# Optimization experiments

Measured on AMD Instinct MI355X. Metric: run time of the kernel, lower is better.

Reference implementation:

```python
import jax, jax.numpy as jnp
import numpy as np

B, N = 64, 4096          # trees per batch, leaves per complete binary tree
V, S = 21, 50            # amino-acid vocab, grammar-symbol vocab
E, H = 64, 128           # embed_dim, hidden_dim


def setup_inputs() -> dict:
    key = jax.random.key(0)
    ks = jax.random.split(key, 16)

    def lin_w(k, din, dout):
        return (jax.random.normal(k, (dout, din), jnp.float32) / np.sqrt(din)).astype(jnp.float32)

    tokens = jax.random.randint(ks[0], (B, N), 0, V, dtype=jnp.int32)
    symbols = jax.random.randint(ks[1], (B, N - 1), 0, S, dtype=jnp.int32)

    emb = jax.random.normal(ks[2], (V, E), jnp.float32) * 0.02
    emb = emb.at[0].set(0.0)  # padding_idx=0
    sym_emb = jax.random.normal(ks[3], (S, E), jnp.float32) * 0.02

    return {
        "tokens": tokens, "symbols": symbols,
        "emb": emb, "sym_emb": sym_emb,
        "Wp": lin_w(ks[4], E, H), "bp": jnp.zeros((H,), jnp.float32),
        "Wi": lin_w(ks[5], H, H), "bi": jnp.zeros((H,), jnp.float32),
        "Ui": lin_w(ks[6], H, H),
        "Wf": lin_w(ks[7], H, H), "bf": jnp.zeros((H,), jnp.float32),
        "Uf": lin_w(ks[8], H, H),
        "Wo": lin_w(ks[9], H, H), "bo": jnp.zeros((H,), jnp.float32),
        "Uo": lin_w(ks[10], H, H),
        "Wu": lin_w(ks[11], H, H), "bu": jnp.zeros((H,), jnp.float32),
        "Uu": lin_w(ks[12], H, H),
        "Wout": lin_w(ks[13], H, H), "bout": jnp.zeros((H,), jnp.float32),
    }


def _encode(tokens, symbols, emb, sym_emb, Wp, bp, Wi, bi, Ui, Wf, bf, Uf,
            Wo, bo, Uo, Wu, bu, Uu, Wout, bout):
    emb = emb.at[0].set(0.0)  # padding row contributes nothing (and gets no grad)

    # Leaf nodes: amino-acid embedding -> input_proj, no children.
    x = emb[tokens] @ Wp.T + bp                      # [B, N, H]
    i = jax.nn.sigmoid(x @ Wi.T + bi)
    o = jax.nn.sigmoid(x @ Wo.T + bo)
    u = jnp.tanh(x @ Wu.T + bu)
    c = i * u                                        # [B, N, H]
    h = o * jnp.tanh(c)

    # Bottom-up over levels of the complete binary tree (Child-Sum Tree-LSTM).
    off, n = 0, N
    while n > 1:
        m = n // 2
        xs = sym_emb[symbols[:, off:off + m]] @ Wp.T + bp   # [B, m, H]
        hl, hr = h[:, 0::2], h[:, 1::2]
        cl, cr = c[:, 0::2], c[:, 1::2]
        ht = hl + hr                                         # h_tilde = sum_j h_j
        gi = jax.nn.sigmoid(xs @ Wi.T + bi + ht @ Ui.T)
        go = jax.nn.sigmoid(xs @ Wo.T + bo + ht @ Uo.T)
        gu = jnp.tanh(xs @ Wu.T + bu + ht @ Uu.T)
        fx = xs @ Wf.T + bf
        fl = jax.nn.sigmoid(fx + hl @ Uf.T)                  # per-child forget gates
        fr = jax.nn.sigmoid(fx + hr @ Uf.T)
        c = gi * gu + fl * cl + fr * cr
        h = go * jnp.tanh(c)
        off += m
        n = m

    root_h = h[:, 0]                                         # [B, H]
    return root_h @ Wout.T + bout                            # output_proj


def reference(tokens, symbols, emb, sym_emb, Wp, bp, Wi, bi, Ui, Wf, bf, Uf,
              Wo, bo, Uo, Wu, bu, Uu, Wout, bout):
    return _encode(tokens, symbols, emb, sym_emb, Wp, bp, Wi, bi, Ui, Wf, bf,
                   Uf, Wo, bo, Uo, Wu, bu, Uu, Wout, bout)
```

## Files before the change

### kernel.cpp

```cpp
#include <hip/hip_runtime.h>
#include <hip/hip_bf16.h>

typedef __attribute__((ext_vector_type(8))) short short8;
typedef __attribute__((ext_vector_type(4))) float f32x4;

static constexpr int B_ = 64;
static constexpr int N_ = 4096;
static constexpr int V_ = 21;
static constexpr int S_ = 50;
static constexpr int E_ = 64;
static constexpr int H_ = 128;
static constexpr int NPAIR = V_ * V_;
static constexpr int NTAB = NPAIR * S_;

__device__ __forceinline__ float rcp_(float x) { return __builtin_amdgcn_rcpf(x); }
__device__ __forceinline__ float sigm(float x) { return rcp_(1.0f + __expf(-x)); }
__device__ __forceinline__ float tanh_(float x) {
  float a = fabsf(x);
  float e = __expf(-2.0f * a);
  float t = (1.0f - e) * rcp_(1.0f + e);
  return x < 0.0f ? -t : t;
}
__device__ __forceinline__ unsigned short f2bf(float f) {
  __hip_bfloat16 b = __float2bfloat16(f);
  return *reinterpret_cast<unsigned short*>(&b);
}
__device__ __forceinline__ float bf2f(unsigned short u) {
  return __uint_as_float(((unsigned int)u) << 16);
}

struct Gates { float cv, hv; };
__device__ __forceinline__ Gates gate_combine(float4 sx,
    float i_p, float o_p, float u_p, float fl_p, float fr_p, float cl, float cr) {
  float gi = sigm(sx.x + i_p);
  float go = sigm(sx.y + o_p);
  float gu = tanh_(sx.z + u_p);
  float fl = sigm(sx.w + fl_p);
  float fr = sigm(sx.w + fr_p);
  float cv = fmaf(gi, gu, fmaf(fl, cl, fr * cr));
  Gates g; g.cv = cv; g.hv = go * tanh_(cv);
  return g;
}

__global__ void __launch_bounds__(512) k_pre0(
    const float* __restrict__ Ui, const float* __restrict__ Uo,
    const float* __restrict__ Uu, const float* __restrict__ Uf,
    const float* __restrict__ Wi, const float* __restrict__ Wo,
    const float* __restrict__ Wu, const float* __restrict__ Wf,
    const float* __restrict__ Wp, const float* __restrict__ Wout,
    unsigned short* __restrict__ Wfrag, float* __restrict__ Wt,
    float* __restrict__ Wxt, float* __restrict__ Wpt,
    float* __restrict__ Woutt) {
  __shared__ float Tt[32][129];
  int blk = blockIdx.x, t = threadIdx.x;
  if (blk < 16) {
    int idx = blk * 512 + t;
    int L = idx & 63;
    int K = (idx >> 6) & 3;
    int T = idx >> 8;
    int n = 16 * T + (L & 15);
    int k0 = 32 * K + ((L >> 4) << 3);
    int g = n >> 7, o = n & 127;
    const float* U = (g == 0) ? Ui : (g == 1) ? Uo : (g == 2) ? Uu : Uf;
    unsigned short out[8];
    #pragma unroll
    for (int j = 0; j < 8; ++j) out[j] = f2bf(U[o * 128 + k0 + j]);
    *(int4*)(Wfrag + (size_t)idx * 8) = *(int4*)out;
  } else if (blk < 48) {
    int job = blk - 16;
    int m = job >> 2, kt = job & 3;
    int k0 = kt * 32;
    const float* M = (m == 0) ? Ui : (m == 1) ? Uo : (m == 2) ? Uu : (m == 3) ? Uf
                   : (m == 4) ? Wi : (m == 5) ? Wo : (m == 6) ? Wu : Wf;
    float* D = (m < 4) ? Wt : Wxt;
    int g = m & 3;
    #pragma unroll
    for (int pass = 0; pass < 2; ++pass) {
      int o = (t >> 3) + 64 * pass;
      int kk = 4 * (t & 7);
      float4 v = *(const float4*)(M + o * 128 + k0 + kk);
      Tt[kk][o] = v.x; Tt[kk + 1][o] = v.y; Tt[kk + 2][o] = v.z; Tt[kk + 3][o] = v.w;
    }
    __syncthreads();
    #pragma unroll
    for (int pass = 0; pass < 8; ++pass) {
      int kk = pass * 4 + (t >> 7);
      int o = t & 127;
      D[(size_t)(k0 + kk) * 512 + g * 128 + o] = Tt[kk][o];
    }
  } else if (blk == 48) {
    for (int i = t; i < E_ * H_; i += 512) {
      int e = i >> 7, o = i & 127;
      Wpt[i] = Wp[o * E_ + e];
    }
  } else {
    for (int i = t; i < H_ * H_; i += 512) {
      int k = i >> 7, o = i & 127;
      Woutt[i] = Wout[o * H_ + k];
    }
  }
}

__global__ void __launch_bounds__(512) k_pre1(
    const float* __restrict__ emb, const float* __restrict__ sym_emb,
    const float* __restrict__ Wpt, const float* __restrict__ Wxt,
    const float* __restrict__ Wt,
    const float* __restrict__ bp, const float* __restrict__ bi,
    const float* __restrict__ bo, const float* __restrict__ bu,
    const float* __restrict__ bfv,
    unsigned short* __restrict__ leaf_h8, float* __restrict__ leaf_c,
    float* __restrict__ symx, float* __restrict__ P_leaf) {
  __shared__ float x[128];
  __shared__ float zs[512];
  __shared__ float hl[128];
  int blk = blockIdx.x, t = threadIdx.x;
  if (blk < V_) {
    int v = blk;
    if (t < 128) {
      float acc = bp[t];
      if (v != 0) {
        for (int e = 0; e < E_; ++e) acc = fmaf(emb[v * E_ + e], Wpt[e * 128 + t], acc);
      }
      x[t] = acc;
    }
    __syncthreads();
    if (t < 384) {
      int g = t >> 7;
      const float* bb = (g == 0) ? bi : (g == 1) ? bo : bu;
      float z = bb[t & 127];
      for (int k = 0; k < H_; ++k) z = fmaf(x[k], Wxt[k * 512 + t], z);
      zs[t] = z;
    }
    __syncthreads();
    if (t < 128) {
      float gi = sigm(zs[t]), go = sigm(zs[128 + t]), gu = tanh_(zs[256 + t]);
      float c = gi * gu;
      leaf_c[v * H_ + t] = c;
      unsigned short hb = f2bf(go * tanh_(c));
      leaf_h8[v * H_ + t] = hb;
      hl[t] = bf2f(hb);
    }
    __syncthreads();
    {
      float z = 0.f;
      for (int k = 0; k < H_; ++k) z = fmaf(hl[k], Wt[k * 512 + t], z);
      P_leaf[(size_t)v * 512 + t] = z;
    }
  } else {
    int s = blk - V_;
    if (t < 128) {
      float acc = bp[t];
      for (int e = 0; e < E_; ++e) acc = fmaf(sym_emb[s * E_ + e], Wpt[e * 128 + t], acc);
      x[t] = acc;
    }
    __syncthreads();
    {
      int g = t >> 7;
      const float* bb = (g == 0) ? bi : (g == 1) ? bo : (g == 2) ? bu : bfv;
      float z = bb[t & 127];
      for (int k = 0; k < H_; ++k) z = fmaf(x[k], Wxt[k * 512 + t], z);
      zs[t] = z;
    }
    __syncthreads();
    if (t < 128) {
      float4 v4 = make_float4(zs[t], zs[128 + t], zs[256 + t], zs[384 + t]);
      *(float4*)(symx + (size_t)s * 512 + t * 4) = v4;
    }
  }
}

__global__ void k_tabB(const float* __restrict__ P_leaf, const float* __restrict__ symx,
                       const float* __restrict__ leaf_c,
                       const int* __restrict__ tokens, const int* __restrict__ symbols,
                       unsigned short* __restrict__ tab_h8, float* __restrict__ tab_c,
                       int* __restrict__ idx1) {
  int blk = blockIdx.x, t = threadIdx.x;
  if (blk < NTAB / 2) {
    int row = blk * 2 + (t >> 7);
    int u = t & 127;
    int p = row / S_, s = row - p * S_;
    int tl = p / V_, tr = p - tl * V_;
    const float* Pl = P_leaf + (size_t)tl * 512;
    const float* Pr = P_leaf + (size_t)tr * 512;
    float4 sx = *(const float4*)(symx + (size_t)s * 512 + u * 4);
    Gates gt = gate_combine(sx,
        Pl[u] + Pr[u], Pl[128 + u] + Pr[128 + u], Pl[256 + u] + Pr[256 + u],
        Pl[384 + u], Pr[384 + u],
        leaf_c[tl * H_ + u], leaf_c[tr * H_ + u]);
    tab_c[(size_t)row * H_ + u] = gt.cv;
    tab_h8[(size_t)row * H_ + u] = f2bf(gt.hv);
  } else {
    int g = (blk - NTAB / 2) * 256 + t;
    int b = g >> 11, j = g & 2047;
    idx1[g] = (tokens[b * N_ + 2 * j] * V_ + tokens[b * N_ + 2 * j + 1]) * S_ + symbols[b * (N_ - 1) + j];
  }
}

__global__ void __launch_bounds__(512, 4) k_lvl23(
    const unsigned short* __restrict__ Wfrag, const float* __restrict__ symx,
    const int* __restrict__ symbols, const int* __restrict__ idx1,
    const unsigned short* __restrict__ gh8, const float* __restrict__ gc,
    unsigned short* __restrict__ h_out8, float* __restrict__ c_out) {
  __shared__ __align__(16) unsigned short Ag[64][136];
  __shared__ __align__(16) unsigned short Bh[32][136];
  __shared__ float Bc[32][132];
  int t = threadIdx.x;
  int w = t >> 6, L = t & 63, q = L >> 4, cL = L & 15;
  int cc = 16 * w + cL;
  int g0 = blockIdx.x * 32;
  int b = g0 >> 10;
  int j2 = g0 & 1023;
  const int* sym_b = symbols + (size_t)b * (N_ - 1);
  const int* gix = idx1 + 2 * g0;

  #pragma unroll
  for (int i = 0; i < 2; ++i) {
    int fid = t + 512 * i;
    int row = fid >> 4, co = (fid & 15) * 8;
    *(int4*)&Ag[row][co] = *(const int4*)(gh8 + (size_t)gix[row] * H_ + co);
  }
  __syncthreads();

  const short8* wf = (const short8*)Wfrag;
  #pragma unroll
  for (int c = 0; c < 2; ++c) {
    float clp[4], crp[4];
    int spre[4];
    #pragma unroll
    for (int it = 0; it < 4; ++it) {
      int n = 16 * c + 8 * (it >> 1) + 2 * q + (it & 1);
      clp[it] = gc[(size_t)gix[2 * n] * H_ + cc];
      crp[it] = gc[(size_t)gix[2 * n + 1] * H_ + cc];
      spre[it] = sym_b[2048 + j2 + n];
    }
    f32x4 acc[2][4];
    #pragma unroll
    for (int r = 0; r < 2; ++r)
      #pragma unroll
      for (int g = 0; g < 4; ++g) acc[r][g] = (f32x4){0.f, 0.f, 0.f, 0.f};
    #pragma unroll
    for (int K = 0; K < 4; ++K) {
      short8 bfr[4];
      #pragma unroll
      for (int g = 0; g < 4; ++g) bfr[g] = wf[(size_t)((w + 8 * g) * 4 + K) * 64 + L];
      short8 a0 = *(const short8*)&Ag[32 * c + cL][K * 32 + q * 8];
      short8 a1 = *(const short8*)&Ag[32 * c + 16 + cL][K * 32 + q * 8];
      #pragma unroll
      for (int g = 0; g < 4; ++g) {
        acc[0][g] = __builtin_amdgcn_mfma_f32_16x16x32_bf16(a0, bfr[g], acc[0][g], 0, 0, 0);
        acc[1][g] = __builtin_amdgcn_mfma_f32_16x16x32_bf16(a1, bfr[g], acc[1][g], 0, 0, 0);
      }
    }
    #pragma unroll
    for (int r = 0; r < 2; ++r) {
      #pragma unroll
      for (int nd = 0; nd < 2; ++nd) {
        int it = r * 2 + nd;
        int n = 16 * c + 8 * r + 2 * q + nd;
        float4 sx = *(const float4*)(symx + (size_t)spre[it] * 512 + cc * 4);
        Gates gt = gate_combine(sx,
            acc[r][0][2 * nd] + acc[r][0][2 * nd + 1],
            acc[r][1][2 * nd] + acc[r][1][2 * nd + 1],
            acc[r][2][2 * nd] + acc[r][2][2 * nd + 1],
            acc[r][3][2 * nd], acc[r][3][2 * nd + 1], clp[it], crp[it]);
        Bc[n][cc] = gt.cv;
        Bh[n][cc] = f2bf(gt.hv);
      }
    }
  }
  __syncthreads();
  {
    int spre[4];
    #pragma unroll
    for (int it = 0; it < 4; ++it) {
      int n = 8 * (it >> 1) + 2 * q + (it & 1);
      spre[it] = sym_b[3072 + (j2 >> 1) + n];
    }
    f32x4 acc[2][4];
    #pragma unroll
    for (int r = 0; r < 2; ++r)
      #pragma unroll
      for (int g = 0; g < 4; ++g) acc[r][g] = (f32x4){0.f, 0.f, 0.f, 0.f};
    #pragma unroll
    for (int K = 0; K < 4; ++K) {
      short8 bfr[4];
      #pragma unroll
      for (int g = 0; g < 4; ++g) bfr[g] = wf[(size_t)((w + 8 * g) * 4 + K) * 64 + L];
      short8 a0 = *(const short8*)&Bh[cL][K * 32 + q * 8];
      short8 a1 = *(const short8*)&Bh[16 + cL][K * 32 + q * 8];
      #pragma unroll
      for (int g = 0; g < 4; ++g) {
        acc[0][g] = __builtin_amdgcn_mfma_f32_16x16x32_bf16(a0, bfr[g], acc[0][g], 0, 0, 0);
        acc[1][g] = __builtin_amdgcn_mfma_f32_16x16x32_bf16(a1, bfr[g], acc[1][g], 0, 0, 0);
      }
    }
    #pragma unroll
    for (int r = 0; r < 2; ++r) {
      #pragma unroll
      for (int nd = 0; nd < 2; ++nd) {
        int it = r * 2 + nd;
        int n = 8 * r + 2 * q + nd;
        int G3 = (g0 >> 1) + n;
        float4 sx = *(const float4*)(symx + (size_t)spre[it] * 512 + cc * 4);
        Gates gt = gate_combine(sx,
            acc[r][0][2 * nd] + acc[r][0][2 * nd + 1],
            acc[r][1][2 * nd] + acc[r][1][2 * nd + 1],
            acc[r][2][2 * nd] + acc[r][2][2 * nd + 1],
            acc[r][3][2 * nd], acc[r][3][2 * nd + 1],
            Bc[2 * n][cc], Bc[2 * n + 1][cc]);
        c_out[(size_t)G3 * H_ + cc] = gt.cv;
        h_out8[(size_t)G3 * H_ + cc] = f2bf(gt.hv);
      }
    }
  }
}

__global__ void __launch_bounds__(512, 2) k_mid(
    const unsigned short* __restrict__ Wfrag, const float* __restrict__ symx,
    const int* __restrict__ symbols,
    const unsigned short* __restrict__ in_h8, const float* __restrict__ in_c,
    unsigned short* __restrict__ out_h8, float* __restrict__ out_c) {
  __shared__ __align__(16) unsigned short Ah0[64][136];
  __shared__ __align__(16) unsigned short Ah1[32][136];
  __shared__ float Cs0[64][128];
  __shared__ float Cs1[32][128];
  int t = threadIdx.x;
  int w = t >> 6, L = t & 63, q = L >> 4, cL = L & 15;
  int cc = 16 * w + cL;
  int blk = blockIdx.x;
  int b = blk >> 3, sub = blk & 7;
  size_t base3 = (size_t)blk * 64;

  #pragma unroll
  for (int i = 0; i < 2; ++i) {
    int fid = t + 512 * i;
    int row = fid >> 4, co = (fid & 15) * 8;
    *(int4*)&Ah0[row][co] = *(const int4*)(in_h8 + (base3 + row) * H_ + co);
  }
  #pragma unroll
  for (int i = 0; i < 4; ++i) {
    int fid = t + 512 * i;
    int row = fid >> 5, c4 = (fid & 31) << 2;
    *(float4*)&Cs0[row][c4] = *(const float4*)(in_c + (base3 + row) * H_ + c4);
  }
  __syncthreads();

  const short8* wf = (const short8*)Wfrag;
  int R = 64;
  #pragma unroll
  for (int lev = 0; lev < 6; ++lev) {
    const int l = 4 + lev;
    const int nodes = R >> 1;
    const int jb = b * (N_ - 1) + (N_ - (N_ >> (l - 1))) + ((sub * 32) >> lev);
    unsigned short (*Ard)[136] = (lev & 1) ? Ah1 : Ah0;
    unsigned short (*Awr)[136] = (lev & 1) ? Ah0 : Ah1;
    const float* crd = (lev & 1) ? &Cs1[0][0] : &Cs0[0][0];
    float* cwr = (lev & 1) ? &Cs0[0][0] : &Cs1[0][0];
    const int nchunk = (nodes + 15) >> 4;
    for (int c = 0; c < nchunk; ++c) {
      int spre[4];
      #pragma unroll
      for (int it = 0; it < 4; ++it) {
        int n = 16 * c + 8 * (it >> 1) + 2 * q + (it & 1);
        spre[it] = (n < nodes) ? symbols[jb + n] : 0;
      }
      f32x4 acc[2][4];
      #pragma unroll
      for (int r = 0; r < 2; ++r)
        #pragma unroll
        for (int g = 0; g < 4; ++g) acc[r][g] = (f32x4){0.f, 0.f, 0.f, 0.f};
      const bool useA1 = (2 * nodes - 32 * c) > 16;
      #pragma unroll
      for (int K = 0; K < 4; ++K) {
        short8 bfr[4];
        #pragma unroll
        for (int g = 0; g < 4; ++g) bfr[g] = wf[(size_t)((w + 8 * g) * 4 + K) * 64 + L];
        short8 a0 = *(const short8*)&Ard[32 * c + cL][K * 32 + q * 8];
        #pragma unroll
        for (int g = 0; g < 4; ++g)
          acc[0][g] = __builtin_amdgcn_mfma_f32_16x16x32_bf16(a0, bfr[g], acc[0][g], 0, 0, 0);
        if (useA1) {
          short8 a1 = *(const short8*)&Ard[32 * c + 16 + cL][K * 32 + q * 8];
          #pragma unroll
          for (int g = 0; g < 4; ++g)
            acc[1][g] = __builtin_amdgcn_mfma_f32_16x16x32_bf16(a1, bfr[g], acc[1][g], 0, 0, 0);
        }
      }
      #pragma unroll
      for (int r = 0; r < 2; ++r) {
        #pragma unroll
        for (int nd = 0; nd < 2; ++nd) {
          int it = r * 2 + nd;
          int n = 16 * c + 8 * r + 2 * q + nd;
          if (n < nodes) {
            float4 sx = *(const float4*)(symx + (size_t)spre[it] * 512 + cc * 4);
            Gates gt = gate_combine(sx,
                acc[r][0][2 * nd] + acc[r][0][2 * nd + 1],
                acc[r][1][2 * nd] + acc[r][1][2 * nd + 1],
                acc[r][2][2 * nd] + acc[r][2][2 * nd + 1],
                acc[r][3][2 * nd], acc[r][3][2 * nd + 1],
                crd[(size_t)(2 * n) * 128 + cc], crd[(size_t)(2 * n + 1) * 128 + cc]);
            if (lev == 5) {
              out_c[(size_t)blk * H_ + cc] = gt.cv;
              out_h8[(size_t)blk * H_ + cc] = f2bf(gt.hv);
            } else {
              cwr[(size_t)n * 128 + cc] = gt.cv;
              Awr[n][cc] = f2bf(gt.hv);
            }
          }
        }
      }
    }
    __syncthreads();
    R >>= 1;
  }
}

__global__ void __launch_bounds__(512, 2) k_fin(
    const unsigned short* __restrict__ Wfrag, const float* __restrict__ symx,
    const int* __restrict__ symbols,
    const unsigned short* __restrict__ in_h8, const float* __restrict__ in_c,
    const float* __restrict__ Woutt, const float* __restrict__ bout,
    float* __restrict__ out) {
  __shared__ __align__(16) unsigned short Ah0[8][136];
  __shared__ __align__(16) unsigned short Ah1[4][136];
  __shared__ float Cs0[8][128];
  __shared__ float Cs1[4][128];
  __shared__ float rootv[128];
  int t = threadIdx.x;
  int w = t >> 6, L = t & 63, q = L >> 4, cL = L & 15;
  int cc = 16 * w + cL;
  int b = blockIdx.x;

  if (t < 128) {
    int row = t >> 4, co = (t & 15) * 8;
    *(int4*)&Ah0[row][co] = *(const int4*)(in_h8 + (size_t)(b * 8 + row) * H_ + co);
  }
  if (t < 256) {
    int row = t >> 5, c4 = (t & 31) << 2;
    *(float4*)&Cs0[row][c4] = *(const float4*)(in_c + (size_t)(b * 8 + row) * H_ + c4);
  }
  __syncthreads();

  const short8* wf = (const short8*)Wfrag;
  int R = 8;
  #pragma unroll
  for (int lev = 0; lev < 3; ++lev) {
    const int l = 10 + lev;
    const int nodes = R >> 1;
    const int jb = b * (N_ - 1) + (N_ - (N_ >> (l - 1)));
    unsigned short (*Ard)[136] = (lev & 1) ? Ah1 : Ah0;
    unsigned short (*Awr)[136] = (lev & 1) ? Ah0 : Ah1;
    const float* crd = (lev & 1) ? &Cs1[0][0] : &Cs0[0][0];
    float* cwr = (lev & 1) ? &Cs0[0][0] : &Cs1[0][0];
    int spre[4];
    #pragma unroll
    for (int it = 0; it < 4; ++it) {
      int n = 8 * (it >> 1) + 2 * q + (it & 1);
      spre[it] = (n < nodes) ? symbols[jb + n] : 0;
    }
    f32x4 acc[4];
    #pragma unroll
    for (int g = 0; g < 4; ++g) acc[g] = (f32x4){0.f, 0.f, 0.f, 0.f};
    #pragma unroll
    for (int K = 0; K < 4; ++K) {
      short8 bfr[4];
      #pragma unroll
      for (int g = 0; g < 4; ++g) bfr[g] = wf[(size_t)((w + 8 * g) * 4 + K) * 64 + L];
      short8 a0 = *(const short8*)&Ard[cL & 7][K * 32 + q * 8];
      #pragma unroll
      for (int g = 0; g < 4; ++g)
        acc[g] = __builtin_amdgcn_mfma_f32_16x16x32_bf16(a0, bfr[g], acc[g], 0, 0, 0);
    }
    #pragma unroll
    for (int nd = 0; nd < 2; ++nd) {
      int it = nd;
      int n = 2 * q + nd;
      if (n < nodes) {
        float4 sx = *(const float4*)(symx + (size_t)spre[it] * 512 + cc * 4);
        Gates gt = gate_combine(sx,
            acc[0][2 * nd] + acc[0][2 * nd + 1],
            acc[1][2 * nd] + acc[1][2 * nd + 1],
            acc[2][2 * nd] + acc[2][2 * nd + 1],
            acc[3][2 * nd], acc[3][2 * nd + 1],
            crd[(size_t)(2 * n) * 128 + cc], crd[(size_t)(2 * n + 1) * 128 + cc]);
        if (lev == 2) {
          rootv[cc] = gt.hv;
        } else {
          cwr[(size_t)n * 128 + cc] = gt.cv;
          Awr[n][cc] = f2bf(gt.hv);
        }
      }
    }
    __syncthreads();
    R >>= 1;
  }
  if (t < 128) {
    float acc = bout[t];
    for (int k = 0; k < H_; ++k) acc = fmaf(rootv[k], Woutt[k * 128 + t], acc);
    out[(size_t)b * H_ + t] = acc;
  }
}

extern "C" void kernel_launch(void* const* d_in, const int* in_sizes, int n_in,
                              void* d_out, int out_size, void* d_ws, size_t ws_size,
                              hipStream_t stream) {
  const int* tokens    = (const int*)d_in[0];
  const int* symbols   = (const int*)d_in[1];
  const float* emb     = (const float*)d_in[2];
  const float* sym_emb = (const float*)d_in[3];
  const float* Wp  = (const float*)d_in[4];
  const float* bp  = (const float*)d_in[5];
  const float* Wi  = (const float*)d_in[6];
  const float* bi  = (const float*)d_in[7];
  const float* Ui  = (const float*)d_in[8];
  const float* Wf  = (const float*)d_in[9];
  const float* bf  = (const float*)d_in[10];
  const float* Uf  = (const float*)d_in[11];
  const float* Wo  = (const float*)d_in[12];
  const float* bo  = (const float*)d_in[13];
  const float* Uo  = (const float*)d_in[14];
  const float* Wu  = (const float*)d_in[15];
  const float* bu  = (const float*)d_in[16];
  const float* Uu  = (const float*)d_in[17];
  const float* Wout= (const float*)d_in[18];
  const float* bout= (const float*)d_in[19];

  char* ws = (char*)d_ws;
  unsigned short* Wfrag   = (unsigned short*)(ws);
  float*          Wt      = (float*)(ws + 131072);
  float*          Wxt     = (float*)(ws + 393216);
  float*          Wpt     = (float*)(ws + 655360);
  float*          Woutt   = (float*)(ws + 688128);
  unsigned short* leaf_h8 = (unsigned short*)(ws + 753664);
  float*          leaf_c  = (float*)(ws + 759040);
  float*          symx    = (float*)(ws + 769792);
  float*          P_leaf  = (float*)(ws + 872192);
  unsigned short* tab_h8  = (unsigned short*)(ws + 2001152UL);
  float*          tab_c   = (float*)(ws + 7645952UL);
  int*            idx1    = (int*)(ws + 18935552UL);
  unsigned short* L3h8    = (unsigned short*)(ws + 19459840UL);
  float*          L3c     = (float*)(ws + 27848448UL);
  unsigned short* L9h8    = (unsigned short*)(ws + 44625664UL);
  float*          L9c     = (float*)(ws + 44756736UL);

  k_pre0<<<50, 512, 0, stream>>>(Ui, Uo, Uu, Uf, Wi, Wo, Wu, Wf, Wp, Wout,
                                 Wfrag, Wt, Wxt, Wpt, Woutt);
  k_pre1<<<V_ + S_, 512, 0, stream>>>(emb, sym_emb, Wpt, Wxt, Wt,
                                      bp, bi, bo, bu, bf,
                                      leaf_h8, leaf_c, symx, P_leaf);
  k_tabB<<<NTAB / 2 + 512, 256, 0, stream>>>(P_leaf, symx, leaf_c, tokens, symbols,
                                             tab_h8, tab_c, idx1);
  k_lvl23<<<2048, 512, 0, stream>>>(Wfrag, symx, symbols, idx1, tab_h8, tab_c, L3h8, L3c);
  k_mid<<<512, 512, 0, stream>>>(Wfrag, symx, symbols, L3h8, L3c, L9h8, L9c);
  k_fin<<<B_, 512, 0, stream>>>(Wfrag, symx, symbols, L9h8, L9c, Woutt, bout,
                                (float*)d_out);
}
```

Measured before the change: 216.2 us.

## Fuse preprocessing and table kernels with grid barrier; merge mid and final levels

Merges the weight-fragment, embedding projection, leaf/symbol precompute, and pair-table kernels into a single kernel that uses an atomic-counter grid barrier between phases. The transposed weight copies are dropped; the weights are read in their original row-major layout. The mid and final tree-level kernels are also merged, with the last 64 blocks waiting on a counter for all 512 blocks before running the top levels. This cuts launches and intermediate buffers, at the cost of spin-wait barriers that assume all blocks are co-resident, less coalesced weight reads, and a raised occupancy hint on the merged kernel.

```diff
diff --git a/kernel.cpp b/kernel.cpp
--- a/kernel.cpp
+++ b/kernel.cpp
@@ -42,19 +42,26 @@
   return g;
 }
 
-__global__ void __launch_bounds__(512) k_pre0(
-    const float* __restrict__ Ui, const float* __restrict__ Uo,
-    const float* __restrict__ Uu, const float* __restrict__ Uf,
-    const float* __restrict__ Wi, const float* __restrict__ Wo,
-    const float* __restrict__ Wu, const float* __restrict__ Wf,
-    const float* __restrict__ Wp, const float* __restrict__ Wout,
-    unsigned short* __restrict__ Wfrag, float* __restrict__ Wt,
-    float* __restrict__ Wxt, float* __restrict__ Wpt,
-    float* __restrict__ Woutt) {
-  __shared__ float Tt[32][129];
+__global__ void __launch_bounds__(256) k_pre_tab(
+    const float* __restrict__ emb, const float* __restrict__ sym_emb,
+    const float* __restrict__ Wp, const float* __restrict__ bp,
+    const float* __restrict__ Wi, const float* __restrict__ bi, const float* __restrict__ Ui,
+    const float* __restrict__ Wf, const float* __restrict__ bfv, const float* __restrict__ Uf,
+    const float* __restrict__ Wo, const float* __restrict__ bo, const float* __restrict__ Uo,
+    const float* __restrict__ Wu, const float* __restrict__ bu, const float* __restrict__ Uu,
+    const int* __restrict__ tokens, const int* __restrict__ symbols,
+    unsigned short* __restrict__ Wfrag,
+    unsigned short* __restrict__ leaf_h8, float* __restrict__ leaf_c,
+    float* __restrict__ symx, float* __restrict__ P_leaf,
+    unsigned short* __restrict__ tab_h8, float* __restrict__ tab_c,
+    int* __restrict__ idx1, unsigned int* __restrict__ ctr) {
+  __shared__ float x[128];
+  __shared__ float zs[512];
+  __shared__ float hsh[128];
   int blk = blockIdx.x, t = threadIdx.x;
-  if (blk < 16) {
-    int idx = blk * 512 + t;
+
+  if (blk < 32) {
+    int idx = blk * 256 + t;
     int L = idx & 63;
     int K = (idx >> 6) & 3;
     int T = idx >> 8;
@@ -66,70 +73,29 @@
     #pragma unroll
     for (int j = 0; j < 8; ++j) out[j] = f2bf(U[o * 128 + k0 + j]);
     *(int4*)(Wfrag + (size_t)idx * 8) = *(int4*)out;
-  } else if (blk < 48) {
-    int job = blk - 16;
-    int m = job >> 2, kt = job & 3;
-    int k0 = kt * 32;
-    const float* M = (m == 0) ? Ui : (m == 1) ? Uo : (m == 2) ? Uu : (m == 3) ? Uf
-                   : (m == 4) ? Wi : (m == 5) ? Wo : (m == 6) ? Wu : Wf;
-    float* D = (m < 4) ? Wt : Wxt;
-    int g = m & 3;
-    #pragma unroll
-    for (int pass = 0; pass < 2; ++pass) {
-      int o = (t >> 3) + 64 * pass;
-      int kk = 4 * (t & 7);
-      float4 v = *(const float4*)(M + o * 128 + k0 + kk);
-      Tt[kk][o] = v.x; Tt[kk + 1][o] = v.y; Tt[kk + 2][o] = v.z; Tt[kk + 3][o] = v.w;
-    }
-    __syncthreads();
-    #pragma unroll
-    for (int pass = 0; pass < 8; ++pass) {
-      int kk = pass * 4 + (t >> 7);
-      int o = t & 127;
-      D[(size_t)(k0 + kk) * 512 + g * 128 + o] = Tt[kk][o];
-    }
-  } else if (blk == 48) {
-    for (int i = t; i < E_ * H_; i += 512) {
-      int e = i >> 7, o = i & 127;
-      Wpt[i] = Wp[o * E_ + e];
-    }
-  } else {
-    for (int i = t; i < H_ * H_; i += 512) {
-      int k = i >> 7, o = i & 127;
-      Woutt[i] = Wout[o * H_ + k];
-    }
-  }
-}
-
-__global__ void __launch_bounds__(512) k_pre1(
-    const float* __restrict__ emb, const float* __restrict__ sym_emb,
-    const float* __restrict__ Wpt, const float* __restrict__ Wxt,
-    const float* __restrict__ Wt,
-    const float* __restrict__ bp, const float* __restrict__ bi,
-    const float* __restrict__ bo, const float* __restrict__ bu,
-    const float* __restrict__ bfv,
-    unsigned short* __restrict__ leaf_h8, float* __restrict__ leaf_c,
-    float* __restrict__ symx, float* __restrict__ P_leaf) {
-  __shared__ float x[128];
-  __shared__ float zs[512];
-  __shared__ float hl[128];
-  int blk = blockIdx.x, t = threadIdx.x;
-  if (blk < V_) {
-    int v = blk;
+  } else if (blk < 53) {
+    int v = blk - 32;
     if (t < 128) {
       float acc = bp[t];
       if (v != 0) {
-        for (int e = 0; e < E_; ++e) acc = fmaf(emb[v * E_ + e], Wpt[e * 128 + t], acc);
+        const float* wr = Wp + t * E_;
+        for (int e = 0; e < E_; ++e) acc = fmaf(emb[v * E_ + e], wr[e], acc);
       }
       x[t] = acc;
     }
     __syncthreads();
-    if (t < 384) {
-      int g = t >> 7;
-      const float* bb = (g == 0) ? bi : (g == 1) ? bo : bu;
-      float z = bb[t & 127];
-      for (int k = 0; k < H_; ++k) z = fmaf(x[k], Wxt[k * 512 + t], z);
-      zs[t] = z;
+    #pragma unroll
+    for (int pp = 0; pp < 2; ++pp) {
+      int col = t + 256 * pp;
+      if (col < 384) {
+        int g = col >> 7, o = col & 127;
+        const float* M = (g == 0) ? Wi : (g == 1) ? Wo : Wu;
+        const float* bb = (g == 0) ? bi : (g == 1) ? bo : bu;
+        float z = bb[o];
+        const float* mr = M + o * H_;
+        for (int k = 0; k < H_; ++k) z = fmaf(x[k], mr[k], z);
+        zs[col] = z;
+      }
     }
     __syncthreads();
     if (t < 128) {
@@ -138,28 +104,38 @@
       leaf_c[v * H_ + t] = c;
       unsigned short hb = f2bf(go * tanh_(c));
       leaf_h8[v * H_ + t] = hb;
-      hl[t] = bf2f(hb);
-    }
-    __syncthreads();
-    {
+      hsh[t] = bf2f(hb);
+    }
+    __syncthreads();
+    #pragma unroll
+    for (int pp = 0; pp < 2; ++pp) {
+      int col = t + 256 * pp;
+      int g = col >> 7, o = col & 127;
+      const float* M = (g == 0) ? Ui : (g == 1) ? Uo : (g == 2) ? Uu : Uf;
       float z = 0.f;
-      for (int k = 0; k < H_; ++k) z = fmaf(hl[k], Wt[k * 512 + t], z);
-      P_leaf[(size_t)v * 512 + t] = z;
-    }
-  } else {
-    int s = blk - V_;
+      const float* mr = M + o * H_;
+      for (int k = 0; k < H_; ++k) z = fmaf(hsh[k], mr[k], z);
+      P_leaf[(size_t)v * 512 + col] = z;
+    }
+  } else if (blk < 103) {
+    int s = blk - 53;
     if (t < 128) {
       float acc = bp[t];
-      for (int e = 0; e < E_; ++e) acc = fmaf(sym_emb[s * E_ + e], Wpt[e * 128 + t], acc);
+      const float* wr = Wp + t * E_;
+      for (int e = 0; e < E_; ++e) acc = fmaf(sym_emb[s * E_ + e], wr[e], acc);
       x[t] = acc;
     }
     __syncthreads();
-    {
-      int g = t >> 7;
+    #pragma unroll
+    for (int pp = 0; pp < 2; ++pp) {
+      int col = t + 256 * pp;
+      int g = col >> 7, o = col & 127;
+      const float* M = (g == 0) ? Wi : (g == 1) ? Wo : (g == 2) ? Wu : Wf;
       const float* bb = (g == 0) ? bi : (g == 1) ? bo : (g == 2) ? bu : bfv;
-      float z = bb[t & 127];
-      for (int k = 0; k < H_; ++k) z = fmaf(x[k], Wxt[k * 512 + t], z);
-      zs[t] = z;
+      float z = bb[o];
+      const float* mr = M + o * H_;
+      for (int k = 0; k < H_; ++k) z = fmaf(x[k], mr[k], z);
+      zs[col] = z;
     }
     __syncthreads();
     if (t < 128) {
@@ -167,32 +143,39 @@
       *(float4*)(symx + (size_t)s * 512 + t * 4) = v4;
     }
   }
-}
-
-__global__ void k_tabB(const float* __restrict__ P_leaf, const float* __restrict__ symx,
-                       const float* __restrict__ leaf_c,
-                       const int* __restrict__ tokens, const int* __restrict__ symbols,
-                       unsigned short* __restrict__ tab_h8, float* __restrict__ tab_c,
-                       int* __restrict__ idx1) {
-  int blk = blockIdx.x, t = threadIdx.x;
-  if (blk < NTAB / 2) {
-    int row = blk * 2 + (t >> 7);
-    int u = t & 127;
-    int p = row / S_, s = row - p * S_;
-    int tl = p / V_, tr = p - tl * V_;
-    const float* Pl = P_leaf + (size_t)tl * 512;
-    const float* Pr = P_leaf + (size_t)tr * 512;
-    float4 sx = *(const float4*)(symx + (size_t)s * 512 + u * 4);
-    Gates gt = gate_combine(sx,
-        Pl[u] + Pr[u], Pl[128 + u] + Pr[128 + u], Pl[256 + u] + Pr[256 + u],
-        Pl[384 + u], Pr[384 + u],
-        leaf_c[tl * H_ + u], leaf_c[tr * H_ + u]);
-    tab_c[(size_t)row * H_ + u] = gt.cv;
-    tab_h8[(size_t)row * H_ + u] = f2bf(gt.hv);
-  } else {
-    int g = (blk - NTAB / 2) * 256 + t;
+
+  {
+    int g = blk * 256 + t;
     int b = g >> 11, j = g & 2047;
-    idx1[g] = (tokens[b * N_ + 2 * j] * V_ + tokens[b * N_ + 2 * j + 1]) * S_ + symbols[b * (N_ - 1) + j];
+    idx1[g] = (tokens[b * N_ + 2 * j] * V_ + tokens[b * N_ + 2 * j + 1]) * S_
+              + symbols[b * (N_ - 1) + j];
+  }
+
+  __syncthreads();
+  __threadfence();
+  if (t == 0) {
+    atomicAdd(ctr, 1u);
+    while (atomicAdd(ctr, 0u) < 512u) __builtin_amdgcn_s_sleep(2);
+  }
+  __syncthreads();
+  __threadfence();
+
+  for (int i = 0; i < 22; ++i) {
+    int row = blk * 2 + i * 1024 + (t >> 7);
+    if (row < NTAB) {
+      int u = t & 127;
+      int p = row / S_, s = row - p * S_;
+      int tl = p / V_, tr = p - tl * V_;
+      const float* Pl = P_leaf + (size_t)tl * 512;
+      const float* Pr = P_leaf + (size_t)tr * 512;
+      float4 sx = *(const float4*)(symx + (size_t)s * 512 + u * 4);
+      Gates gt = gate_combine(sx,
+          Pl[u] + Pr[u], Pl[128 + u] + Pr[128 + u], Pl[256 + u] + Pr[256 + u],
+          Pl[384 + u], Pr[384 + u],
+          leaf_c[tl * H_ + u], leaf_c[tr * H_ + u]);
+      tab_c[(size_t)row * H_ + u] = gt.cv;
+      tab_h8[(size_t)row * H_ + u] = f2bf(gt.hv);
+    }
   }
 }
 
@@ -315,11 +298,13 @@
   }
 }
 
-__global__ void __launch_bounds__(512, 2) k_mid(
+__global__ void __launch_bounds__(512, 4) k_midfin(
     const unsigned short* __restrict__ Wfrag, const float* __restrict__ symx,
     const int* __restrict__ symbols,
     const unsigned short* __restrict__ in_h8, const float* __restrict__ in_c,
-    unsigned short* __restrict__ out_h8, float* __restrict__ out_c) {
+    unsigned short* __restrict__ l9_h8, float* __restrict__ l9_c,
+    const float* __restrict__ Wout, const float* __restrict__ bout,
+    float* __restrict__ out, unsigned int* __restrict__ ctr) {
   __shared__ __align__(16) unsigned short Ah0[64][136];
   __shared__ __align__(16) unsigned short Ah1[32][136];
   __shared__ float Cs0[64][128];
@@ -401,8 +386,8 @@
                 acc[r][3][2 * nd], acc[r][3][2 * nd + 1],
                 crd[(size_t)(2 * n) * 128 + cc], crd[(size_t)(2 * n + 1) * 128 + cc]);
             if (lev == 5) {
-              out_c[(size_t)blk * H_ + cc] = gt.cv;
-              out_h8[(size_t)blk * H_ + cc] = f2bf(gt.hv);
+              l9_c[(size_t)blk * H_ + cc] = gt.cv;
+              l9_h8[(size_t)blk * H_ + cc] = f2bf(gt.hv);
             } else {
               cwr[(size_t)n * 128 + cc] = gt.cv;
               Awr[n][cc] = f2bf(gt.hv);
@@ -414,91 +399,86 @@
     __syncthreads();
     R >>= 1;
   }
-}
-
-__global__ void __launch_bounds__(512, 2) k_fin(
-    const unsigned short* __restrict__ Wfrag, const float* __restrict__ symx,
-    const int* __restrict__ symbols,
-    const unsigned short* __restrict__ in_h8, const float* __restrict__ in_c,
-    const float* __restrict__ Woutt, const float* __restrict__ bout,
-    float* __restrict__ out) {
-  __shared__ __align__(16) unsigned short Ah0[8][136];
-  __shared__ __align__(16) unsigned short Ah1[4][136];
-  __shared__ float Cs0[8][128];
-  __shared__ float Cs1[4][128];
-  __shared__ float rootv[128];
-  int t = threadIdx.x;
-  int w = t >> 6, L = t & 63, q = L >> 4, cL = L & 15;
-  int cc = 16 * w + cL;
-  int b = blockIdx.x;
-
-  if (t < 128) {
-    int row = t >> 4, co = (t & 15) * 8;
-    *(int4*)&Ah0[row][co] = *(const int4*)(in_h8 + (size_t)(b * 8 + row) * H_ + co);
-  }
-  if (t < 256) {
-    int row = t >> 5, c4 = (t & 31) << 2;
-    *(float4*)&Cs0[row][c4] = *(const float4*)(in_c + (size_t)(b * 8 + row) * H_ + c4);
+
+  __threadfence();
+  if (t == 0) atomicAdd(ctr, 1u);
+  if (blk >= 64) return;
+  if (t == 0) {
+    while (atomicAdd(ctr, 0u) < 512u) __builtin_amdgcn_s_sleep(2);
   }
   __syncthreads();
-
-  const short8* wf = (const short8*)Wfrag;
-  int R = 8;
-  #pragma unroll
-  for (int lev = 0; lev < 3; ++lev) {
-    const int l = 10 + lev;
-    const int nodes = R >> 1;
-    const int jb = b * (N_ - 1) + (N_ - (N_ >> (l - 1)));
-    unsigned short (*Ard)[136] = (lev & 1) ? Ah1 : Ah0;
-    unsigned short (*Awr)[136] = (lev & 1) ? Ah0 : Ah1;
-    const float* crd = (lev & 1) ? &Cs1[0][0] : &Cs0[0][0];
-    float* cwr = (lev & 1) ? &Cs0[0][0] : &Cs1[0][0];
-    int spre[4];
-    #pragma unroll
-    for (int it = 0; it < 4; ++it) {
-      int n = 8 * (it >> 1) + 2 * q + (it & 1);
-      spre[it] = (n < nodes) ? symbols[jb + n] : 0;
-    }
-    f32x4 acc[4];
-    #pragma unroll
-    for (int g = 0; g < 4; ++g) acc[g] = (f32x4){0.f, 0.f, 0.f, 0.f};
-    #pragma unroll
-    for (int K = 0; K < 4; ++K) {
-      short8 bfr[4];
-      #pragma unroll
-      for (int g = 0; g < 4; ++g) bfr[g] = wf[(size_t)((w + 8 * g) * 4 + K) * 64 + L];
-      short8 a0 = *(const short8*)&Ard[cL & 7][K * 32 + q * 8];
-      #pragma unroll
-      for (int g = 0; g < 4; ++g)
-        acc[g] = __builtin_amdgcn_mfma_f32_16x16x32_bf16(a0, bfr[g], acc[g], 0, 0, 0);
-    }
-    #pragma unroll
-    for (int nd = 0; nd < 2; ++nd) {
-      int it = nd;
-      int n = 2 * q + nd;
-      if (n < nodes) {
-        float4 sx = *(const float4*)(symx + (size_t)spre[it] * 512 + cc * 4);
-        Gates gt = gate_combine(sx,
-            acc[0][2 * nd] + acc[0][2 * nd + 1],
-            acc[1][2 * nd] + acc[1][2 * nd + 1],
-            acc[2][2 * nd] + acc[2][2 * nd + 1],
-            acc[3][2 * nd], acc[3][2 * nd + 1],
-            crd[(size_t)(2 * n) * 128 + cc], crd[(size_t)(2 * n + 1) * 128 + cc]);
-        if (lev == 2) {
-          rootv[cc] = gt.hv;
-        } else {
-          cwr[(size_t)n * 128 + cc] = gt.cv;
-          Awr[n][cc] = f2bf(gt.hv);
+  __threadfence();
+
+  {
+    int fb = blk;
+    float* rootv = &Cs0[32][0];
+    if (t < 128) {
+      int row = t >> 4, co = (t & 15) * 8;
+      *(int4*)&Ah0[row][co] = *(const int4*)(l9_h8 + (size_t)(fb * 8 + row) * H_ + co);
+    }
+    if (t < 256) {
+      int row = t >> 5, c4 = (t & 31) << 2;
+      *(float4*)&Cs0[row][c4] = *(const float4*)(l9_c + (size_t)(fb * 8 + row) * H_ + c4);
+    }
+    __syncthreads();
+
+    int R2 = 8;
+    #pragma unroll
+    for (int lev = 0; lev < 3; ++lev) {
+      const int l = 10 + lev;
+      const int nodes = R2 >> 1;
+      const int jb = fb * (N_ - 1) + (N_ - (N_ >> (l - 1)));
+      unsigned short (*Ard)[136] = (lev & 1) ? Ah1 : Ah0;
+      unsigned short (*Awr)[136] = (lev & 1) ? Ah0 : Ah1;
+      const float* crd = (lev & 1) ? &Cs1[0][0] : &Cs0[0][0];
+      float* cwr = (lev & 1) ? &Cs0[0][0] : &Cs1[0][0];
+      int spre[2];
+      #pragma unroll
+      for (int it = 0; it < 2; ++it) {
+        int n = 2 * q + it;
+        spre[it] = (n < nodes) ? symbols[jb + n] : 0;
+      }
+      f32x4 acc[4];
+      #pragma unroll
+      for (int g = 0; g < 4; ++g) acc[g] = (f32x4){0.f, 0.f, 0.f, 0.f};
+      #pragma unroll
+      for (int K = 0; K < 4; ++K) {
+        short8 bfr[4];
+        #pragma unroll
+        for (int g = 0; g < 4; ++g) bfr[g] = wf[(size_t)((w + 8 * g) * 4 + K) * 64 + L];
+        short8 a0 = *(const short8*)&Ard[cL & 7][K * 32 + q * 8];
+        #pragma unroll
+        for (int g = 0; g < 4; ++g)
+          acc[g] = __builtin_amdgcn_mfma_f32_16x16x32_bf16(a0, bfr[g], acc[g], 0, 0, 0);
+      }
+      #pragma unroll
+      for (int nd = 0; nd < 2; ++nd) {
+        int n = 2 * q + nd;
+        if (n < nodes) {
+          float4 sx = *(const float4*)(symx + (size_t)spre[nd] * 512 + cc * 4);
+          Gates gt = gate_combine(sx,
+              acc[0][2 * nd] + acc[0][2 * nd + 1],
+              acc[1][2 * nd] + acc[1][2 * nd + 1],
+              acc[2][2 * nd] + acc[2][2 * nd + 1],
+              acc[3][2 * nd], acc[3][2 * nd + 1],
+              crd[(size_t)(2 * n) * 128 + cc], crd[(size_t)(2 * n + 1) * 128 + cc]);
+          if (lev == 2) {
+            rootv[cc] = gt.hv;
+          } else {
+            cwr[(size_t)n * 128 + cc] = gt.cv;
+            Awr[n][cc] = f2bf(gt.hv);
+          }
         }
       }
-    }
-    __syncthreads();
-    R >>= 1;
-  }
-  if (t < 128) {
-    float acc = bout[t];
-    for (int k = 0; k < H_; ++k) acc = fmaf(rootv[k], Woutt[k * 128 + t], acc);
-    out[(size_t)b * H_ + t] = acc;
+      __syncthreads();
+      R2 >>= 1;
+    }
+    if (t < 128) {
+      float acc = bout[t];
+      const float* wr = Wout + t * H_;
+      for (int k = 0; k < H_; ++k) acc = fmaf(rootv[k], wr[k], acc);
+      out[(size_t)fb * H_ + t] = acc;
+    }
   }
 }
 
@@ -527,32 +507,27 @@
   const float* bout= (const float*)d_in[19];
 
   char* ws = (char*)d_ws;
-  unsigned short* Wfrag   = (unsigned short*)(ws);
-  float*          Wt      = (float*)(ws + 131072);
-  float*          Wxt     = (float*)(ws + 393216);
-  float*          Wpt     = (float*)(ws + 655360);
-  float*          Woutt   = (float*)(ws + 688128);
-  unsigned short* leaf_h8 = (unsigned short*)(ws + 753664);
-  float*          leaf_c  = (float*)(ws + 759040);
-  float*          symx    = (float*)(ws + 769792);
-  float*          P_leaf  = (float*)(ws + 872192);
-  unsigned short* tab_h8  = (unsigned short*)(ws + 2001152UL);
-  float*          tab_c   = (float*)(ws + 7645952UL);
-  int*            idx1    = (int*)(ws + 18935552UL);
-  unsigned short* L3h8    = (unsigned short*)(ws + 19459840UL);
-  float*          L3c     = (float*)(ws + 27848448UL);
-  unsigned short* L9h8    = (unsigned short*)(ws + 44625664UL);
-  float*          L9c     = (float*)(ws + 44756736UL);
-
-  k_pre0<<<50, 512, 0, stream>>>(Ui, Uo, Uu, Uf, Wi, Wo, Wu, Wf, Wp, Wout,
-                                 Wfrag, Wt, Wxt, Wpt, Woutt);
-  k_pre1<<<V_ + S_, 512, 0, stream>>>(emb, sym_emb, Wpt, Wxt, Wt,
-                                      bp, bi, bo, bu, bf,
-                                      leaf_h8, leaf_c, symx, P_leaf);
-  k_tabB<<<NTAB / 2 + 512, 256, 0, stream>>>(P_leaf, symx, leaf_c, tokens, symbols,
-                                             tab_h8, tab_c, idx1);
-  k_lvl23<<<2048, 512, 0, stream>>>(Wfrag, symx, symbols, idx1, tab_h8, tab_c, L3h8, L3c);
-  k_mid<<<512, 512, 0, stream>>>(Wfrag, symx, symbols, L3h8, L3c, L9h8, L9c);
-  k_fin<<<B_, 512, 0, stream>>>(Wfrag, symx, symbols, L9h8, L9c, Woutt, bout,
-                                (float*)d_out);
-}
+  unsigned int*   ctrs    = (unsigned int*)(ws);
+  unsigned short* Wfrag   = (unsigned short*)(ws + 256);
+  unsigned short* leaf_h8 = (unsigned short*)(ws + 131328);
+  float*          leaf_c  = (float*)(ws + 136704);
+  float*          symx    = (float*)(ws + 147456);
+  float*          P_leaf  = (float*)(ws + 249856);
+  unsigned short* tab_h8  = (unsigned short*)(ws + 292864);
+  float*          tab_c   = (float*)(ws + 5937664UL);
+  int*            idx1    = (int*)(ws + 17227264UL);
+  unsigned short* L3h8    = (unsigned short*)(ws + 17751552UL);
+  float*          L3c     = (float*)(ws + 26140160UL);
+  unsigned short* L9h8    = (unsigned short*)(ws + 42917376UL);
+  float*          L9c     = (float*)(ws + 43048448UL);
+
+  hipMemsetAsync(ctrs, 0, 16, stream);
+  k_pre_tab<<<512, 256, 0, stream>>>(emb, sym_emb, Wp, bp,
+      Wi, bi, Ui, Wf, bf, Uf, Wo, bo, Uo, Wu, bu, Uu,
+      tokens, symbols, Wfrag, leaf_h8, leaf_c, symx, P_leaf,
+      tab_h8, tab_c, idx1, ctrs);
+  k_lvl23<<<2048, 512, 0, stream>>>(Wfrag, symx, symbols, idx1, tab_h8, tab_c,
+                                    L3h8, L3c);
+  k_midfin<<<512, 512, 0, stream>>>(Wfrag, symx, symbols, L3h8, L3c,
+                                    L9h8, L9c, Wout, bout, (float*)d_out, ctrs + 2);
+}
```

New measurement: 384.0 us. +77.6%, slower.

## Fuse two more tree levels into first level kernel, shift mid/fin stages up

Applied to the files above, without the earlier changes.

The first level kernel now also computes levels 4 and 5 in shared memory, reusing its LDS buffers for intermediate h/c, and writes level-5 outputs instead of level-3. The mid kernel processes levels 6-11 with 128 blocks instead of 512, and the final kernel handles only the root level. This removes a large global write/read of level-3 intermediates, at the cost of lower parallelism in k_mid (128 blocks) and extra serial MFMA work per block in the first kernel.

```diff
diff --git a/kernel.cpp b/kernel.cpp
--- a/kernel.cpp
+++ b/kernel.cpp
@@ -196,7 +196,7 @@
   }
 }
 
-__global__ void __launch_bounds__(512, 4) k_lvl23(
+__global__ void __launch_bounds__(512, 4) k_l25(
     const unsigned short* __restrict__ Wfrag, const float* __restrict__ symx,
     const int* __restrict__ symbols, const int* __restrict__ idx1,
     const unsigned short* __restrict__ gh8, const float* __restrict__ gc,
@@ -204,6 +204,7 @@
   __shared__ __align__(16) unsigned short Ag[64][136];
   __shared__ __align__(16) unsigned short Bh[32][136];
   __shared__ float Bc[32][132];
+  float* c3p = (float*)&Ag[16][0];
   int t = threadIdx.x;
   int w = t >> 6, L = t & 63, q = L >> 4, cL = L & 15;
   int cc = 16 * w + cL;
@@ -300,7 +301,6 @@
       for (int nd = 0; nd < 2; ++nd) {
         int it = r * 2 + nd;
         int n = 8 * r + 2 * q + nd;
-        int G3 = (g0 >> 1) + n;
         float4 sx = *(const float4*)(symx + (size_t)spre[it] * 512 + cc * 4);
         Gates gt = gate_combine(sx,
             acc[r][0][2 * nd] + acc[r][0][2 * nd + 1],
@@ -308,8 +308,81 @@
             acc[r][2][2 * nd] + acc[r][2][2 * nd + 1],
             acc[r][3][2 * nd], acc[r][3][2 * nd + 1],
             Bc[2 * n][cc], Bc[2 * n + 1][cc]);
-        c_out[(size_t)G3 * H_ + cc] = gt.cv;
-        h_out8[(size_t)G3 * H_ + cc] = f2bf(gt.hv);
+        c3p[(size_t)n * 128 + cc] = gt.cv;
+        Ag[n][cc] = f2bf(gt.hv);
+      }
+    }
+  }
+  __syncthreads();
+  {
+    int spre[2];
+    #pragma unroll
+    for (int it = 0; it < 2; ++it) {
+      int n = 2 * q + it;
+      spre[it] = sym_b[3584 + (j2 >> 2) + n];
+    }
+    f32x4 acc[4];
+    #pragma unroll
+    for (int g = 0; g < 4; ++g) acc[g] = (f32x4){0.f, 0.f, 0.f, 0.f};
+    #pragma unroll
+    for (int K = 0; K < 4; ++K) {
+      short8 bfr[4];
+      #pragma unroll
+      for (int g = 0; g < 4; ++g) bfr[g] = wf[(size_t)((w + 8 * g) * 4 + K) * 64 + L];
+      short8 a0 = *(const short8*)&Ag[cL][K * 32 + q * 8];
+      #pragma unroll
+      for (int g = 0; g < 4; ++g)
+        acc[g] = __builtin_amdgcn_mfma_f32_16x16x32_bf16(a0, bfr[g], acc[g], 0, 0, 0);
+    }
+    #pragma unroll
+    for (int nd = 0; nd < 2; ++nd) {
+      int n = 2 * q + nd;
+      float4 sx = *(const float4*)(symx + (size_t)spre[nd] * 512 + cc * 4);
+      Gates gt = gate_combine(sx,
+          acc[0][2 * nd] + acc[0][2 * nd + 1],
+          acc[1][2 * nd] + acc[1][2 * nd + 1],
+          acc[2][2 * nd] + acc[2][2 * nd + 1],
+          acc[3][2 * nd], acc[3][2 * nd + 1],
+          c3p[(size_t)(2 * n) * 128 + cc], c3p[(size_t)(2 * n + 1) * 128 + cc]);
+      Bc[n][cc] = gt.cv;
+      Bh[n][cc] = f2bf(gt.hv);
+    }
+  }
+  __syncthreads();
+  {
+    int spre[2];
+    #pragma unroll
+    for (int it = 0; it < 2; ++it) {
+      int n = 2 * q + it;
+      spre[it] = (n < 4) ? sym_b[3840 + (j2 >> 3) + n] : 0;
+    }
+    f32x4 acc[4];
+    #pragma unroll
+    for (int g = 0; g < 4; ++g) acc[g] = (f32x4){0.f, 0.f, 0.f, 0.f};
+    #pragma unroll
+    for (int K = 0; K < 4; ++K) {
+      short8 bfr[4];
+      #pragma unroll
+      for (int g = 0; g < 4; ++g) bfr[g] = wf[(size_t)((w + 8 * g) * 4 + K) * 64 + L];
+      short8 a0 = *(const short8*)&Bh[cL][K * 32 + q * 8];
+      #pragma unroll
+      for (int g = 0; g < 4; ++g)
+        acc[g] = __builtin_amdgcn_mfma_f32_16x16x32_bf16(a0, bfr[g], acc[g], 0, 0, 0);
+    }
+    #pragma unroll
+    for (int nd = 0; nd < 2; ++nd) {
+      int n = 2 * q + nd;
+      if (n < 4) {
+        float4 sx = *(const float4*)(symx + (size_t)spre[nd] * 512 + cc * 4);
+        Gates gt = gate_combine(sx,
+            acc[0][2 * nd] + acc[0][2 * nd + 1],
+            acc[1][2 * nd] + acc[1][2 * nd + 1],
+            acc[2][2 * nd] + acc[2][2 * nd + 1],
+            acc[3][2 * nd], acc[3][2 * nd + 1],
+            Bc[2 * n][cc], Bc[2 * n + 1][cc]);
+        int G5 = blockIdx.x * 4 + n;
+        c_out[(size_t)G5 * H_ + cc] = gt.cv;
+        h_out8[(size_t)G5 * H_ + cc] = f2bf(gt.hv);
       }
     }
   }
@@ -328,20 +401,20 @@
   int w = t >> 6, L = t & 63, q = L >> 4, cL = L & 15;
   int cc = 16 * w + cL;
   int blk = blockIdx.x;
-  int b = blk >> 3, sub = blk & 7;
-  size_t base3 = (size_t)blk * 64;
+  int b = blk >> 1, sub = blk & 1;
+  size_t base5 = (size_t)blk * 64;
 
   #pragma unroll
   for (int i = 0; i < 2; ++i) {
     int fid = t + 512 * i;
     int row = fid >> 4, co = (fid & 15) * 8;
-    *(int4*)&Ah0[row][co] = *(const int4*)(in_h8 + (base3 + row) * H_ + co);
+    *(int4*)&Ah0[row][co] = *(const int4*)(in_h8 + (base5 + row) * H_ + co);
   }
   #pragma unroll
   for (int i = 0; i < 4; ++i) {
     int fid = t + 512 * i;
     int row = fid >> 5, c4 = (fid & 31) << 2;
-    *(float4*)&Cs0[row][c4] = *(const float4*)(in_c + (base3 + row) * H_ + c4);
+    *(float4*)&Cs0[row][c4] = *(const float4*)(in_c + (base5 + row) * H_ + c4);
   }
   __syncthreads();
 
@@ -349,7 +422,7 @@
   int R = 64;
   #pragma unroll
   for (int lev = 0; lev < 6; ++lev) {
-    const int l = 4 + lev;
+    const int l = 6 + lev;
     const int nodes = R >> 1;
     const int jb = b * (N_ - 1) + (N_ - (N_ >> (l - 1))) + ((sub * 32) >> lev);
     unsigned short (*Ard)[136] = (lev & 1) ? Ah1 : Ah0;
@@ -422,83 +495,56 @@
     const unsigned short* __restrict__ in_h8, const float* __restrict__ in_c,
     const float* __restrict__ Woutt, const float* __restrict__ bout,
     float* __restrict__ out) {
-  __shared__ __align__(16) unsigned short Ah0[8][136];
-  __shared__ __align__(16) unsigned short Ah1[4][136];
-  __shared__ float Cs0[8][128];
-  __shared__ float Cs1[4][128];
+  __shared__ __align__(16) unsigned short Ah[16][136];
+  __shared__ float Cs[2][128];
   __shared__ float rootv[128];
   int t = threadIdx.x;
   int w = t >> 6, L = t & 63, q = L >> 4, cL = L & 15;
   int cc = 16 * w + cL;
   int b = blockIdx.x;
 
+  if (t < 32) {
+    int row = t >> 4, co = (t & 15) * 8;
+    *(int4*)&Ah[row][co] = *(const int4*)(in_h8 + (size_t)(b * 2 + row) * H_ + co);
+  } else if (t < 256) {
+    int fid = t - 32;
+    int row = 2 + (fid >> 4), co = (fid & 15) * 8;
+    int4 z = {0, 0, 0, 0};
+    *(int4*)&Ah[row][co] = z;
+  }
+  if (t < 64) {
+    int row = t >> 5, c4 = (t & 31) << 2;
+    *(float4*)&Cs[row][c4] = *(const float4*)(in_c + (size_t)(b * 2 + row) * H_ + c4);
+  }
+  __syncthreads();
+
+  const short8* wf = (const short8*)Wfrag;
+  int s12 = symbols[b * (N_ - 1) + 4094];
+  f32x4 acc[4];
+  #pragma unroll
+  for (int g = 0; g < 4; ++g) acc[g] = (f32x4){0.f, 0.f, 0.f, 0.f};
+  #pragma unroll
+  for (int K = 0; K < 4; ++K) {
+    short8 bfr[4];
+    #pragma unroll
+    for (int g = 0; g < 4; ++g) bfr[g] = wf[(size_t)((w + 8 * g) * 4 + K) * 64 + L];
+    short8 a0 = *(const short8*)&Ah[cL][K * 32 + q * 8];
+    #pragma unroll
+    for (int g = 0; g < 4; ++g)
+      acc[g] = __builtin_amdgcn_mfma_f32_16x16x32_bf16(a0, bfr[g], acc[g], 0, 0, 0);
+  }
+  if (q == 0) {
+    float4 sx = *(const float4*)(symx + (size_t)s12 * 512 + cc * 4);
+    Gates gt = gate_combine(sx,
+        acc[0][0] + acc[0][1], acc[1][0] + acc[1][1], acc[2][0] + acc[2][1],
+        acc[3][0], acc[3][1], Cs[0][cc], Cs[1][cc]);
+    rootv[cc] = gt.hv;
+  }
+  __syncthreads();
   if (t < 128) {
-    int row = t >> 4, co = (t & 15) * 8;
-    *(int4*)&Ah0[row][co] = *(const int4*)(in_h8 + (size_t)(b * 8 + row) * H_ + co);
-  }
-  if (t < 256) {
-    int row = t >> 5, c4 = (t & 31) << 2;
-    *(float4*)&Cs0[row][c4] = *(const float4*)(in_c + (size_t)(b * 8 + row) * H_ + c4);
-  }
-  __syncthreads();
-
-  const short8* wf = (const short8*)Wfrag;
-  int R = 8;
-  #pragma unroll
-  for (int lev = 0; lev < 3; ++lev) {
-    const int l = 10 + lev;
-    const int nodes = R >> 1;
-    const int jb = b * (N_ - 1) + (N_ - (N_ >> (l - 1)));
-    unsigned short (*Ard)[136] = (lev & 1) ? Ah1 : Ah0;
-    unsigned short (*Awr)[136] = (lev & 1) ? Ah0 : Ah1;
-    const float* crd = (lev & 1) ? &Cs1[0][0] : &Cs0[0][0];
-    float* cwr = (lev & 1) ? &Cs0[0][0] : &Cs1[0][0];
-    int spre[4];
-    #pragma unroll
-    for (int it = 0; it < 4; ++it) {
-      int n = 8 * (it >> 1) + 2 * q + (it & 1);
-      spre[it] = (n < nodes) ? symbols[jb + n] : 0;
-    }
-    f32x4 acc[4];
-    #pragma unroll
-    for (int g = 0; g < 4; ++g) acc[g] = (f32x4){0.f, 0.f, 0.f, 0.f};
-    #pragma unroll
-    for (int K = 0; K < 4; ++K) {
-      short8 bfr[4];
-      #pragma unroll
-      for (int g = 0; g < 4; ++g) bfr[g] = wf[(size_t)((w + 8 * g) * 4 + K) * 64 + L];
-      short8 a0 = *(const short8*)&Ard[cL & 7][K * 32 + q * 8];
-      #pragma unroll
-      for (int g = 0; g < 4; ++g)
-        acc[g] = __builtin_amdgcn_mfma_f32_16x16x32_bf16(a0, bfr[g], acc[g], 0, 0, 0);
-    }
-    #pragma unroll
-    for (int nd = 0; nd < 2; ++nd) {
-      int it = nd;
-      int n = 2 * q + nd;
-      if (n < nodes) {
-        float4 sx = *(const float4*)(symx + (size_t)spre[it] * 512 + cc * 4);
-        Gates gt = gate_combine(sx,
-            acc[0][2 * nd] + acc[0][2 * nd + 1],
-            acc[1][2 * nd] + acc[1][2 * nd + 1],
-            acc[2][2 * nd] + acc[2][2 * nd + 1],
-            acc[3][2 * nd], acc[3][2 * nd + 1],
-            crd[(size_t)(2 * n) * 128 + cc], crd[(size_t)(2 * n + 1) * 128 + cc]);
-        if (lev == 2) {
-          rootv[cc] = gt.hv;
-        } else {
-          cwr[(size_t)n * 128 + cc] = gt.cv;
-          Awr[n][cc] = f2bf(gt.hv);
-        }
-      }
-    }
-    __syncthreads();
-    R >>= 1;
-  }
-  if (t < 128) {
-    float acc = bout[t];
-    for (int k = 0; k < H_; ++k) acc = fmaf(rootv[k], Woutt[k * 128 + t], acc);
-    out[(size_t)b * H_ + t] = acc;
+    float acc2 = bout[t];
+    for (int k = 0; k < H_; ++k) acc2 = fmaf(rootv[k], Woutt[k * 128 + t], acc2);
+    out[(size_t)b * H_ + t] = acc2;
   }
 }
 
@@ -536,13 +582,13 @@
   float*          leaf_c  = (float*)(ws + 759040);
   float*          symx    = (float*)(ws + 769792);
   float*          P_leaf  = (float*)(ws + 872192);
-  unsigned short* tab_h8  = (unsigned short*)(ws + 2001152UL);
-  float*          tab_c   = (float*)(ws + 7645952UL);
-  int*            idx1    = (int*)(ws + 18935552UL);
-  unsigned short* L3h8    = (unsigned short*)(ws + 19459840UL);
-  float*          L3c     = (float*)(ws + 27848448UL);
-  unsigned short* L9h8    = (unsigned short*)(ws + 44625664UL);
-  float*          L9c     = (float*)(ws + 44756736UL);
+  unsigned short* tab_h8  = (unsigned short*)(ws + 915200);
+  float*          tab_c   = (float*)(ws + 6560000UL);
+  int*            idx1    = (int*)(ws + 17849600UL);
+  unsigned short* L5h8    = (unsigned short*)(ws + 18373888UL);
+  float*          L5c     = (float*)(ws + 20471040UL);
+  unsigned short* L11h8   = (unsigned short*)(ws + 24665344UL);
+  float*          L11c    = (float*)(ws + 24698112UL);
 
   k_pre0<<<50, 512, 0, stream>>>(Ui, Uo, Uu, Uf, Wi, Wo, Wu, Wf, Wp, Wout,
                                  Wfrag, Wt, Wxt, Wpt, Woutt);
@@ -551,8 +597,9 @@
                                       leaf_h8, leaf_c, symx, P_leaf);
   k_tabB<<<NTAB / 2 + 512, 256, 0, stream>>>(P_leaf, symx, leaf_c, tokens, symbols,
                                              tab_h8, tab_c, idx1);
-  k_lvl23<<<2048, 512, 0, stream>>>(Wfrag, symx, symbols, idx1, tab_h8, tab_c, L3h8, L3c);
-  k_mid<<<512, 512, 0, stream>>>(Wfrag, symx, symbols, L3h8, L3c, L9h8, L9c);
-  k_fin<<<B_, 512, 0, stream>>>(Wfrag, symx, symbols, L9h8, L9c, Woutt, bout,
+  k_l25<<<2048, 512, 0, stream>>>(Wfrag, symx, symbols, idx1, tab_h8, tab_c,
+                                  L5h8, L5c);
+  k_mid<<<128, 512, 0, stream>>>(Wfrag, symx, symbols, L5h8, L5c, L11h8, L11c);
+  k_fin<<<B_, 512, 0, stream>>>(Wfrag, symx, symbols, L11h8, L11c, Woutt, bout,
                                 (float*)d_out);
 }
```

New measurement: 226.3 us. 4.6% more time.
